# Performance work log

Hardware: AMD Instinct MI355X
Metric: run time of the kernel (lower is better)

Reference implementation:

```python
import jax, jax.numpy as jnp
import numpy as np

N_NODES = 6000
DEG = 16
N_EDGES = N_NODES * DEG
D_MODEL = 256
D_MSG = 64
D_FF = 4 * D_MODEL
N_LAYERS = 3
N_SPECIES = 108
RBF_BINS = D_MODEL
RBF_VMIN, RBF_VMAX = 0.0, 8.0


def setup_inputs():
    key = jax.random.key(0)
    ks = jax.random.split(key, 16)
    rng = np.random.default_rng(0)
    # graph: each node i has DEG in-edges (dst block-structured), random sources
    atomic_number = jnp.asarray(rng.integers(1, N_SPECIES, N_NODES), dtype=jnp.int32)
    dst = np.repeat(np.arange(N_NODES), DEG)
    src = rng.integers(0, N_NODES, N_EDGES)
    # angle graph t: nodes = edges of g; edges = all ordered pairs of in-edges sharing dst
    pq = np.array([(p, q) for p in range(DEG) for q in range(DEG) if p != q], dtype=np.int64)
    off = (np.arange(N_NODES) * DEG)[:, None]
    t_src = (off + pq[:, 0][None, :]).reshape(-1)
    t_dst = (off + pq[:, 1][None, :]).reshape(-1)
    r = jax.random.normal(ks[0], (N_EDGES, 3), dtype=jnp.float32) * 2.0  # bond vectors, |r|~3A
    s_dm = 1.0 / np.sqrt(D_MODEL)
    s_dmsg = 1.0 / np.sqrt(D_MSG)
    s_ff = 1.0 / np.sqrt(D_FF)
    return {
        'r': r,
        'atomic_number': atomic_number,
        'src': jnp.asarray(src, dtype=jnp.int32),
        'dst': jnp.asarray(dst, dtype=jnp.int32),
        't_src': jnp.asarray(t_src, dtype=jnp.int32),
        't_dst': jnp.asarray(t_dst, dtype=jnp.int32),
        'emb': jax.random.normal(ks[1], (N_SPECIES, D_MODEL), dtype=jnp.float32),
        'Wsrc': jax.random.normal(ks[2], (N_LAYERS, D_MSG, D_MODEL), dtype=jnp.float32) * s_dm,
        'bsrc': jnp.zeros((N_LAYERS, D_MSG), jnp.float32),
        'Wdst': jax.random.normal(ks[3], (N_LAYERS, D_MSG, D_MODEL), dtype=jnp.float32) * s_dm,
        'bdst': jnp.zeros((N_LAYERS, D_MSG), jnp.float32),
        'Wedge': jax.random.normal(ks[4], (N_LAYERS, D_MSG, D_MODEL), dtype=jnp.float32) * s_dm,
        'bedge': jnp.zeros((N_LAYERS, D_MSG), jnp.float32),
        'attn': jax.random.normal(ks[5], (N_LAYERS, D_MSG), dtype=jnp.float32) * s_dmsg,
        'W1': jax.random.normal(ks[6], (N_LAYERS, D_FF, D_MSG), dtype=jnp.float32) * s_dmsg,
        'b1': jnp.zeros((N_LAYERS, D_FF), jnp.float32),
        'W2': jax.random.normal(ks[7], (N_LAYERS, D_MODEL, D_FF), dtype=jnp.float32) * s_ff,
        'b2': jnp.zeros((N_LAYERS, D_MODEL), jnp.float32),
        'Wfc': jax.random.normal(ks[8], (1, D_MODEL), dtype=jnp.float32) * s_dm,
        'bfc': jnp.zeros((1,), jnp.float32),
    }


def _segment_softmax(logits, seg, num):
    m = jax.ops.segment_max(logits, seg, num_segments=num)
    ex = jnp.exp(logits - m[seg])
    z = jax.ops.segment_sum(ex, seg, num_segments=num)
    return ex / z[seg]


def reference(r, atomic_number, src, dst, t_src, t_dst, emb, Wsrc, bsrc, Wdst, bdst,
              Wedge, bedge, attn, W1, b1, W2, b2, Wfc, bfc):
    x = emb[atomic_number]                                   # [N, d_model]
    d = jnp.linalg.norm(r, axis=1)                           # [E]
    centers = jnp.linspace(RBF_VMIN, RBF_VMAX, RBF_BINS, dtype=r.dtype)
    gamma = 1.0 / (centers[1] - centers[0])
    y = jnp.exp(-gamma * (d[:, None] - centers[None, :]) ** 2)  # [E, d_model]
    rhat = r / d[:, None]
    # cos angle between edge pairs (sign of -r cancels in u_dot_v)
    cos_jik = jnp.clip(jnp.sum(rhat[t_src] * rhat[t_dst], axis=1), -1.0 + 1e-6, 1.0 - 1e-6)
    nch = jnp.arange(D_MSG, dtype=r.dtype)
    z_jik = jnp.cos(nch[None, :] * jnp.arccos(cos_jik)[:, None])  # Chebyshev T_k(cos) [T, 64]
    for l in range(N_LAYERS):
        xj = x @ Wsrc[l].T + bsrc[l]                          # [N, 64]
        xi = x @ Wdst[l].T + bdst[l]
        xij = xj[src] + xi[dst] + (y @ Wedge[l].T + bedge[l])  # [E, 64]
        e_jik = jax.nn.silu(z_jik + xij[t_src] + xij[t_dst])   # [T, 64]
        logits = e_jik @ attn[l]                               # [T]
        a = _segment_softmax(logits, t_dst, N_EDGES)           # edge_softmax over angle graph
        ft = jax.ops.segment_sum(a[:, None] * xij[t_src], t_dst, num_segments=N_EDGES)  # [E, 64]
        xn = jax.ops.segment_sum(ft, dst, num_segments=N_NODES)  # scatter to nodes [N, 64]
        x = jax.nn.silu(xn @ W1[l].T + b1[l]) @ W2[l].T + b2[l]  # FFN -> [N, d_model]
    atomwise = x @ Wfc.T + bfc                                  # [N, 1]
    return jnp.squeeze(jnp.mean(atomwise, axis=0))              # AvgPooling (eV/atom)


if __name__ == '__main__':
    out = reference(**setup_inputs())
    print(out)
```

## Files before the change

### kernel.cpp

```cpp
#include <hip/hip_runtime.h>

#define N_NODES 6000
#define DEG_    16
#define N_EDGES (N_NODES*DEG_)
#define D_MODEL 256
#define D_MSG   64
#define D_FF    1024

typedef __bf16 bf16x8 __attribute__((ext_vector_type(8)));
typedef float floatx4 __attribute__((ext_vector_type(4)));

__device__ __forceinline__ float silu_f(float v) {
    return v * __builtin_amdgcn_rcpf(1.0f + __expf(-v));
}
__device__ __forceinline__ float b2f(unsigned short u) {
    union { unsigned int i; float f; } v; v.i = ((unsigned int)u) << 16; return v.f;
}
__device__ __forceinline__ unsigned short f2b(float f) {
    union { float f; unsigned int i; } v; v.f = f;
    unsigned int r = (v.i + 0x7FFFu + ((v.i >> 16) & 1u)) >> 16;
    return (unsigned short)r;
}

#define WSRC_OFF 0
#define WDST_OFF 49152
#define WCVT_TOTAL 98304
#define CVT4_BLOCKS (WCVT_TOTAL/4/256)
#define EMB4_BLOCKS (N_NODES*D_MODEL/4/256)
#define GEOM_BLOCKS (N_EDGES/256)
#define WPACKE_BLOCKS 24
#define WPACK1_BLOCKS 96
__global__ __launch_bounds__(256) void prep_kernel(
    const float* __restrict__ Wsrc, const float* __restrict__ Wdst,
    const float* __restrict__ Wedge, const float* __restrict__ W1,
    unsigned short* __restrict__ wbf_out,
    const int* __restrict__ an, const float* __restrict__ emb,
    unsigned short* __restrict__ x,
    const float* __restrict__ r, float* __restrict__ d, float* __restrict__ rhat,
    unsigned short* __restrict__ wedgep,
    unsigned short* __restrict__ w1p) {
    int b = blockIdx.x;
    int t = threadIdx.x;
    if (b < CVT4_BLOCKS) {
        int i = (b*256 + t) * 4;
        const float* sp = (i < WDST_OFF) ? (Wsrc + i) : (Wdst + (i - WDST_OFF));
        float4 v = *(const float4*)sp;
        *(ushort4*)(wbf_out + i) = make_ushort4(f2b(v.x), f2b(v.y), f2b(v.z), f2b(v.w));
    } else if (b < CVT4_BLOCKS + EMB4_BLOCKS) {
        int i4 = (b - CVT4_BLOCKS)*256 + t;
        int node = i4 >> 6, c4 = i4 & 63;
        float4 v = *(const float4*)(emb + (size_t)an[node]*D_MODEL + c4*4);
        *(ushort4*)(x + (size_t)node*D_MODEL + c4*4) =
            make_ushort4(f2b(v.x), f2b(v.y), f2b(v.z), f2b(v.w));
    } else if (b < CVT4_BLOCKS + EMB4_BLOCKS + GEOM_BLOCKS) {
        int e = (b - CVT4_BLOCKS - EMB4_BLOCKS)*256 + t;
        float xx = r[e*3+0], yy = r[e*3+1], zz = r[e*3+2];
        float n = sqrtf(xx*xx + yy*yy + zz*zz);
        d[e] = n;
        float inv = 1.0f / n;
        *(float4*)(rhat + (size_t)e*4) = make_float4(xx*inv, yy*inv, zz*inv, 0.f);
    } else if (b < CVT4_BLOCKS + EMB4_BLOCKS + GEOM_BLOCKS + WPACKE_BLOCKS) {
        int wb = b - (CVT4_BLOCKS + EMB4_BLOCKS + GEOM_BLOCKS);
        int i = wb*256 + t;
        int lane = i & 63, ks = (i >> 6) & 7, rem = i >> 9;
        int ns = rem % 3, w = rem / 3;
        int row = 48*w + ns*16 + (lane & 15);
        int col = ks*32 + (lane >> 4)*8;
        const float* sp = Wedge + (size_t)row*256 + col;
        float4 v0 = *(const float4*)sp;
        float4 v1 = *(const float4*)(sp + 4);
        unsigned short h[8] = { f2b(v0.x), f2b(v0.y), f2b(v0.z), f2b(v0.w),
                                f2b(v1.x), f2b(v1.y), f2b(v1.z), f2b(v1.w) };
        *(uint4*)(wedgep + (size_t)i*8) = *(uint4*)h;
    } else {
        int wb = b - (CVT4_BLOCKS + EMB4_BLOCKS + GEOM_BLOCKS + WPACKE_BLOCKS);
        int i2 = wb*256 + t;
        int lp = i2 >> 13;
        int e = i2 & 8191;
        int lane = e & 63, j = (e >> 6) & 1, wv = (e >> 7) & 3, f = e >> 9;
        int row = f*64 + wv*16 + (lane & 15);
        int col = j*32 + (lane >> 4)*8;
        const float* sp = W1 + (size_t)lp*65536 + (size_t)row*64 + col;
        float4 v0 = *(const float4*)sp;
        float4 v1 = *(const float4*)(sp + 4);
        unsigned short h[8] = { f2b(v0.x), f2b(v0.y), f2b(v0.z), f2b(v0.w),
                                f2b(v1.x), f2b(v1.y), f2b(v1.z), f2b(v1.w) };
        *(uint4*)(w1p + (size_t)i2*8) = *(uint4*)h;
    }
}

#define EPITCH 264
#define APITCH 40
#define MCP 72
__global__ __launch_bounds__(256) void eplg_kernel(
    const unsigned short* __restrict__ Bwp,
    const float* __restrict__ bias,
    const float* __restrict__ dvec,
    unsigned short* __restrict__ C,
    const unsigned short* __restrict__ A,
    const unsigned short* __restrict__ B1g,
    const unsigned short* __restrict__ B2g,
    const float* __restrict__ bias1,
    const float* __restrict__ bias2,
    unsigned short* __restrict__ Cg,
    const float* __restrict__ Wsrc, const float* __restrict__ Wdst,
    const float* __restrict__ W2, const float* __restrict__ b2,
    const float* __restrict__ Wfc, const float* __restrict__ bfc,
    unsigned short* __restrict__ wcomb,
    float* __restrict__ bcomb,
    float* __restrict__ wfc2,
    float* __restrict__ out) {
    __shared__ __align__(16) unsigned short sm[64*EPITCH];
    const int t = threadIdx.x;
    const int w = t >> 6, lane = t & 63, lr = lane & 15, lq = lane >> 4;

    if (blockIdx.x < 1500) {
        unsigned short* As = sm;
        const int m0 = blockIdx.x * 64;
        const int arow = t >> 2, achk = t & 3;

        float dv = dvec[m0 + arow];
        const float gamma = 31.875f;
        const float step  = 8.0f / 255.0f;
        #pragma unroll
        for (int c32 = 0; c32 < 8; ++c32) {
            int kb = c32*32 + achk*8;
            unsigned short h[8];
            #pragma unroll
            for (int j = 0; j < 8; ++j) {
                float tt = dv - (float)(kb+j)*step;
                h[j] = f2b(__expf(-gamma*tt*tt));
            }
            *(uint4*)(&As[arow*EPITCH + kb]) = *(uint4*)h;
        }
        __syncthreads();

        const unsigned short* Bp = Bwp + (size_t)w*12288 + lane*8;

        floatx4 acc[4][3] = {};
        uint4 pb[3];
        #pragma unroll
        for (int ns = 0; ns < 3; ++ns)
            pb[ns] = *(const uint4*)(Bp + ns*4096);

        for (int k0 = 0; k0 < 256; k0 += 32) {
            int ks = k0 >> 5;
            uint4 cb[3];
            cb[0] = pb[0]; cb[1] = pb[1]; cb[2] = pb[2];
            if (k0 + 32 < 256) {
                #pragma unroll
                for (int ns = 0; ns < 3; ++ns)
                    pb[ns] = *(const uint4*)(Bp + ns*4096 + (ks+1)*512);
            }
            bf16x8 af[4];
            #pragma unroll
            for (int mi = 0; mi < 4; ++mi)
                af[mi] = *(const bf16x8*)(&As[(mi*16 + lr)*EPITCH + k0 + lq*8]);
            #pragma unroll
            for (int mi = 0; mi < 4; ++mi) {
                #pragma unroll
                for (int ns = 0; ns < 3; ++ns)
                    acc[mi][ns] = __builtin_amdgcn_mfma_f32_16x16x32_bf16(
                        af[mi], *(const bf16x8*)&cb[ns], acc[mi][ns], 0, 0, 0);
            }
        }

        #pragma unroll
        for (int ns = 0; ns < 3; ++ns) {
            int bc = 48*w + ns*16 + lr;
            float bv = bias[bc];
            #pragma unroll
            for (int mi = 0; mi < 4; ++mi) {
                #pragma unroll
                for (int rg = 0; rg < 4; ++rg) {
                    int row = m0 + mi*16 + lq*4 + rg;
                    C[(size_t)row*192 + bc] = f2b(acc[mi][ns][rg] + bv);
                }
            }
        }
        return;
    }
    if (blockIdx.x < 1688) {
        unsigned short* As = sm;
        unsigned short* Bs = sm + 2560;
        unsigned short* Cs = sm;
        const int bid2 = blockIdx.x - 1500;
        const int bx = bid2 & 1;
        const int m0 = (bid2 >> 1) * 64;
        const unsigned short* B = bx ? B2g : B1g;
        const float* biasl = bx ? bias2 : bias1;
        const int n0 = bx * 64;
        const int K = 256, M = N_NODES, lda = 256, ldb = 256, ldc = 128;

        const int arow = t >> 2, achk = t & 3;

        floatx4 acc[4] = {};
        uint4 pa, pb;
        {
            int gm = m0 + arow;
            pa = (gm < M) ? *(const uint4*)(A + (size_t)gm*lda + achk*8) : make_uint4(0,0,0,0);
        }
        pb = *(const uint4*)(B + (size_t)arow*ldb + achk*8);

        for (int k0 = 0; k0 < K; k0 += 32) {
            *(uint4*)(&As[arow*APITCH + achk*8]) = pa;
            *(uint4*)(&Bs[arow*APITCH + achk*8]) = pb;
            __syncthreads();
            if (k0 + 32 < K) {
                int kn = k0 + 32;
                int gm = m0 + arow;
                pa = (gm < M) ? *(const uint4*)(A + (size_t)gm*lda + kn + achk*8) : make_uint4(0,0,0,0);
                pb = *(const uint4*)(B + (size_t)arow*ldb + kn + achk*8);
            }
            bf16x8 af, bfr[4];
            af = *(const bf16x8*)(&As[(w*16 + lr)*APITCH + lq*8]);
            #pragma unroll
            for (int ns = 0; ns < 4; ++ns)
                bfr[ns] = *(const bf16x8*)(&Bs[(ns*16 + lr)*APITCH + lq*8]);
            #pragma unroll
            for (int ns = 0; ns < 4; ++ns)
                acc[ns] = __builtin_amdgcn_mfma_f32_16x16x32_bf16(af, bfr[ns], acc[ns], 0,0,0);
            __syncthreads();
        }
        #pragma unroll
        for (int ns = 0; ns < 4; ++ns) {
            int bc = ns*16 + lr;
            float bv = biasl[bc];
            #pragma unroll
            for (int rg = 0; rg < 4; ++rg) {
                int lrow = w*16 + lq*4 + rg;
                Cs[lrow*MCP + bc] = f2b(acc[ns][rg] + bv);
            }
        }
        __syncthreads();
        #pragma unroll
        for (int it = 0; it < 2; ++it) {
            int i = t + it*256;
            int row = i >> 3, c8 = i & 7;
            int gm = m0 + row;
            if (gm < M)
                *(uint4*)(Cg + (size_t)gm*ldc + n0 + c8*8) = *(const uint4*)(Cs + row*MCP + c8*8);
        }
        return;
    }
    {
        int b = blockIdx.x - 1688;
        if (b < 64) {
            int lp  = 1 + (b >> 5);
            int wb2 = b & 31;
            const float* W2f = W2 + (size_t)(lp-1)*262144;
            const float* wm[4];
            #pragma unroll
            for (int i = 0; i < 4; ++i) {
                int row = wb2*4 + i;
                wm[i] = (row < 64) ? (Wsrc + (size_t)lp*16384 + row*256)
                                   : (Wdst + (size_t)lp*16384 + (row-64)*256);
            }
            float acc[4][4] = {};
            int c0 = t*4;
            #pragma unroll 8
            for (int c = 0; c < 256; ++c) {
                float4 w2v = *(const float4*)(W2f + (size_t)c*1024 + c0);
                #pragma unroll
                for (int i = 0; i < 4; ++i) {
                    float wv2 = wm[i][c];
                    acc[i][0] = fmaf(wv2, w2v.x, acc[i][0]);
                    acc[i][1] = fmaf(wv2, w2v.y, acc[i][1]);
                    acc[i][2] = fmaf(wv2, w2v.z, acc[i][2]);
                    acc[i][3] = fmaf(wv2, w2v.w, acc[i][3]);
                }
            }
            int fc = t >> 4, j = (t >> 3) & 1, lq2 = (t >> 1) & 3, cpos = (t & 1) * 4;
            #pragma unroll
            for (int i = 0; i < 4; ++i) {
                int row = wb2*4 + i;
                int wv2 = row >> 5, ns = (row >> 4) & 1, lr2 = row & 15;
                *(ushort4*)(wcomb + (size_t)(lp-1)*131072
                            + (size_t)fc*8192 + wv2*2048 + ns*1024 + j*512 + (lq2*16+lr2)*8 + cpos) =
                    make_ushort4(f2b(acc[i][0]), f2b(acc[i][1]), f2b(acc[i][2]), f2b(acc[i][3]));
            }
        } else if (b < 68) {
            int c = (b - 64)*256 + t;
            const float* W2f = W2 + 2*262144;
            float a0 = 0.f, a1 = 0.f, a2 = 0.f, a3 = 0.f;
            #pragma unroll 4
            for (int k = 0; k < 256; k += 4) {
                a0 = fmaf(Wfc[k+0], W2f[(size_t)(k+0)*1024 + c], a0);
                a1 = fmaf(Wfc[k+1], W2f[(size_t)(k+1)*1024 + c], a1);
                a2 = fmaf(Wfc[k+2], W2f[(size_t)(k+2)*1024 + c], a2);
                a3 = fmaf(Wfc[k+3], W2f[(size_t)(k+3)*1024 + c], a3);
            }
            wfc2[c] = (a0 + a1) + (a2 + a3);
        } else {
            int lp = 1 + (t >> 7);
            int row = t & 127;
            const float* b2l = b2 + (lp-1)*256;
            const float* wmrow = (row < 64) ? (Wsrc + (size_t)lp*16384 + row*256)
                                            : (Wdst + (size_t)lp*16384 + (row-64)*256);
            float acc = 0.f;
            #pragma unroll 8
            for (int c = 0; c < 256; ++c) acc += wmrow[c] * b2l[c];
            acc += (row < 64) ? bias1[lp*64 + row] : bias2[lp*64 + (row-64)];
            bcomb[(lp-1)*128 + row] = acc;
            if (t == 0) {
                float bo = 0.f;
                const float* b23 = b2 + 2*256;
                #pragma unroll 8
                for (int c = 0; c < 256; ++c) bo += Wfc[c] * b23[c];
                out[0] = bo + bfc[0];
            }
        }
    }
}

#define HP 72
#define CP2 136
__global__ __launch_bounds__(256) void ffw_kernel(
    const unsigned short* __restrict__ XN,
    const unsigned short* __restrict__ W1p,
    const float* __restrict__ b1l,
    const unsigned short* __restrict__ WCp,
    const float* __restrict__ bcl,
    unsigned short* __restrict__ XO,
    int M) {
    __shared__ __align__(16) unsigned short s_h[16*HP];
    __shared__ __align__(16) unsigned short s_c[16*CP2];
    const int t = threadIdx.x;
    const int wv = t >> 6, lane = t & 63, lr = lane & 15, lq = lane >> 4;
    const int m0 = blockIdx.x * 16;

    int ga = m0 + lr;
    bool aok = ga < M;
    uint4 a0 = aok ? *(const uint4*)(XN + (size_t)ga*64 + lq*8) : make_uint4(0,0,0,0);
    uint4 a1 = aok ? *(const uint4*)(XN + (size_t)ga*64 + 32 + lq*8) : make_uint4(0,0,0,0);

    floatx4 acc2[2] = {};

    const unsigned short* W1b = W1p + (size_t)wv*1024 + lane*8;
    const unsigned short* WCb = WCp + (size_t)wv*2048 + lane*8;

    uint4 pb1[2], pb2[4];
    pb1[0] = *(const uint4*)(W1b);
    pb1[1] = *(const uint4*)(W1b + 512);
    pb2[0] = *(const uint4*)(WCb);
    pb2[1] = *(const uint4*)(WCb + 512);
    pb2[2] = *(const uint4*)(WCb + 1024);
    pb2[3] = *(const uint4*)(WCb + 1536);

    for (int f = 0; f < 16; ++f) {
        uint4 cb1_0 = pb1[0], cb1_1 = pb1[1];
        uint4 cb2_0 = pb2[0], cb2_1 = pb2[1], cb2_2 = pb2[2], cb2_3 = pb2[3];
        float bv1 = b1l[f*64 + wv*16 + lr];
        if (f < 15) {
            const unsigned short* n1 = W1b + (f+1)*4096;
            const unsigned short* n2 = WCb + (f+1)*8192;
            pb1[0] = *(const uint4*)(n1);
            pb1[1] = *(const uint4*)(n1 + 512);
            pb2[0] = *(const uint4*)(n2);
            pb2[1] = *(const uint4*)(n2 + 512);
            pb2[2] = *(const uint4*)(n2 + 1024);
            pb2[3] = *(const uint4*)(n2 + 1536);
        }
        floatx4 hacc = {};
        hacc = __builtin_amdgcn_mfma_f32_16x16x32_bf16(
            *(const bf16x8*)&a0, *(const bf16x8*)&cb1_0, hacc, 0,0,0);
        hacc = __builtin_amdgcn_mfma_f32_16x16x32_bf16(
            *(const bf16x8*)&a1, *(const bf16x8*)&cb1_1, hacc, 0,0,0);
        {
            int col = wv*16 + lr;
            #pragma unroll
            for (int rg = 0; rg < 4; ++rg) {
                int row = lq*4 + rg;
                s_h[row*HP + col] = f2b(silu_f(hacc[rg] + bv1));
            }
        }
        __syncthreads();
        bf16x8 ha0 = *(const bf16x8*)(&s_h[lr*HP + lq*8]);
        bf16x8 ha1 = *(const bf16x8*)(&s_h[lr*HP + 32 + lq*8]);
        acc2[0] = __builtin_amdgcn_mfma_f32_16x16x32_bf16(ha0, *(const bf16x8*)&cb2_0, acc2[0], 0,0,0);
        acc2[0] = __builtin_amdgcn_mfma_f32_16x16x32_bf16(ha1, *(const bf16x8*)&cb2_1, acc2[0], 0,0,0);
        acc2[1] = __builtin_amdgcn_mfma_f32_16x16x32_bf16(ha0, *(const bf16x8*)&cb2_2, acc2[1], 0,0,0);
        acc2[1] = __builtin_amdgcn_mfma_f32_16x16x32_bf16(ha1, *(const bf16x8*)&cb2_3, acc2[1], 0,0,0);
        __syncthreads();
    }

    #pragma unroll
    for (int ns = 0; ns < 2; ++ns) {
        int col = wv*32 + ns*16 + lr;
        float bv = bcl[col];
        #pragma unroll
        for (int rg = 0; rg < 4; ++rg) {
            int row = lq*4 + rg;
            s_c[row*CP2 + col] = f2b(acc2[ns][rg] + bv);
        }
    }
    __syncthreads();
    {
        int row = t >> 4, c8 = t & 15;
        int gm = m0 + row;
        if (gm < M)
            *(uint4*)(XO + (size_t)gm*128 + c8*8) = *(const uint4*)(s_c + row*CP2 + c8*8);
    }
}

__global__ __launch_bounds__(256) void ffa_kernel(
    const unsigned short* __restrict__ XN,
    const unsigned short* __restrict__ W1p,
    const float* __restrict__ b1l,
    const float* __restrict__ wfc2,
    float* __restrict__ out, int M) {
    __shared__ float red[256];
    const int t = threadIdx.x;
    const int wv = t >> 6, lane = t & 63, lr = lane & 15, lq = lane >> 4;
    const int m0 = blockIdx.x * 16;

    int ga = m0 + lr;
    bool aok = ga < M;
    uint4 a0 = aok ? *(const uint4*)(XN + (size_t)ga*64 + lq*8) : make_uint4(0,0,0,0);
    uint4 a1 = aok ? *(const uint4*)(XN + (size_t)ga*64 + 32 + lq*8) : make_uint4(0,0,0,0);

    const unsigned short* W1b = W1p + (size_t)wv*1024 + lane*8;
    uint4 pb0 = *(const uint4*)(W1b);
    uint4 pb1 = *(const uint4*)(W1b + 512);

    float partial = 0.f;
    for (int f = 0; f < 16; ++f) {
        uint4 c0 = pb0, c1 = pb1;
        if (f < 15) {
            pb0 = *(const uint4*)(W1b + (f+1)*4096);
            pb1 = *(const uint4*)(W1b + (f+1)*4096 + 512);
        }
        floatx4 hacc = {};
        hacc = __builtin_amdgcn_mfma_f32_16x16x32_bf16(
            *(const bf16x8*)&a0, *(const bf16x8*)&c0, hacc, 0,0,0);
        hacc = __builtin_amdgcn_mfma_f32_16x16x32_bf16(
            *(const bf16x8*)&a1, *(const bf16x8*)&c1, hacc, 0,0,0);
        float bv1 = b1l[f*64 + wv*16 + lr];
        float wvv = wfc2[f*64 + wv*16 + lr];
        #pragma unroll
        for (int rg = 0; rg < 4; ++rg) {
            int gm = m0 + lq*4 + rg;
            if (gm < M) partial += silu_f(hacc[rg] + bv1) * wvv;
        }
    }
    red[t] = partial;
    __syncthreads();
    for (int off = 128; off > 0; off >>= 1) {
        if (t < off) red[t] += red[t+off];
        __syncthreads();
    }
    if (t == 0) atomicAdd(out, red[0] * (1.0f/(float)N_NODES));
}

__global__ __launch_bounds__(256) void angle_kernel(
    const unsigned short* __restrict__ xjxi,
    const unsigned short* __restrict__ eproj,
    const float* __restrict__ rhat,
    const int*   __restrict__ src,
    const float* __restrict__ attn,
    unsigned short* __restrict__ xn) {
    __shared__ __align__(16) float s_xij[16][68];
    __shared__ float s_rhat[16][4];
    __shared__ float s_logit[16][17];
    __shared__ float s_a[16][17];
    __shared__ float s_w[16];
    const int tt = threadIdx.x;
    const int node = blockIdx.x;

    if (tt < 16) {
        float4 rv = *(const float4*)(rhat + (size_t)(node*DEG_ + tt)*4);
        s_rhat[tt][0] = rv.x; s_rhat[tt][1] = rv.y; s_rhat[tt][2] = rv.z; s_rhat[tt][3] = 0.f;
        s_logit[tt][tt] = -1e30f;
    }
    {
        int p = tt >> 4, c4 = tt & 15;
        int e = node*DEG_ + p;
        int se = src[e];
        ushort4 aj = *(const ushort4*)(xjxi + (size_t)se*128 + c4*4);
        ushort4 ai = *(const ushort4*)(xjxi + (size_t)node*128 + 64 + c4*4);
        ushort4 ae = *(const ushort4*)(eproj + (size_t)e*192 + c4*4);
        s_xij[p][c4*4+0] = b2f(aj.x) + b2f(ai.x) + b2f(ae.x);
        s_xij[p][c4*4+1] = b2f(aj.y) + b2f(ai.y) + b2f(ae.y);
        s_xij[p][c4*4+2] = b2f(aj.z) + b2f(ai.z) + b2f(ae.z);
        s_xij[p][c4*4+3] = b2f(aj.w) + b2f(ai.w) + b2f(ae.w);
    }
    __syncthreads();
    int pp = 0, qq = 0;
    float lg = 0.f;
    if (tt < 240) {
        int pair = tt >> 1, half = tt & 1;
        pp = (int)((1.0f + sqrtf(8.0f*(float)pair + 1.0f)) * 0.5f);
        qq = pair - ((pp*(pp-1)) >> 1);
        float c = s_rhat[pp][0]*s_rhat[qq][0] + s_rhat[pp][1]*s_rhat[qq][1]
                + s_rhat[pp][2]*s_rhat[qq][2];
        c = fminf(fmaxf(c, -0.999999f), 0.999999f);
        float c2 = 2.0f * c;
        float tk0, tk1;
        if (half) {
            float T2  = fmaf(c2, c, -1.0f);
            float T3  = fmaf(2.0f*T2,  c,   -c);
            float T4  = fmaf(2.0f*T2,  T2,  -1.0f);
            float T7  = fmaf(2.0f*T4,  T3,  -c);
            float T8  = fmaf(2.0f*T4,  T4,  -1.0f);
            float T15 = fmaf(2.0f*T8,  T7,  -c);
            float T16 = fmaf(2.0f*T8,  T8,  -1.0f);
            float T31 = fmaf(2.0f*T16, T15, -c);
            float T32 = fmaf(2.0f*T16, T16, -1.0f);
            float T33 = fmaf(2.0f*T32, c,   -T31);
            tk0 = T32; tk1 = T33;
        } else {
            tk0 = 1.0f; tk1 = c;
        }
        const float* xp = &s_xij[pp][0] + half*32;
        const float* xq = &s_xij[qq][0] + half*32;
        const float* at = attn + half*32;
        float acc = 0.f;
        #pragma unroll
        for (int k0 = 0; k0 < 32; k0 += 4) {
            float4 xp4 = *(const float4*)(xp + k0);
            float4 xq4 = *(const float4*)(xq + k0);
            float a0 = at[k0+0], a1 = at[k0+1], a2 = at[k0+2], a3 = at[k0+3];
            float v0 = tk0 + xp4.x + xq4.x;
            acc = fmaf(a0, silu_f(v0), acc);
            { float tn2 = c2*tk1 - tk0; tk0 = tk1; tk1 = tn2; }
            float v1 = tk0 + xp4.y + xq4.y;
            acc = fmaf(a1, silu_f(v1), acc);
            { float tn2 = c2*tk1 - tk0; tk0 = tk1; tk1 = tn2; }
            float v2 = tk0 + xp4.z + xq4.z;
            acc = fmaf(a2, silu_f(v2), acc);
            { float tn2 = c2*tk1 - tk0; tk0 = tk1; tk1 = tn2; }
            float v3 = tk0 + xp4.w + xq4.w;
            acc = fmaf(a3, silu_f(v3), acc);
            { float tn2 = c2*tk1 - tk0; tk0 = tk1; tk1 = tn2; }
        }
        lg = acc;
    }
    lg += __shfl_xor(lg, 1);
    if (tt < 240 && (tt & 1) == 0) {
        s_logit[pp][qq] = lg;
        s_logit[qq][pp] = lg;
    }
    __syncthreads();
    {
        int q = tt >> 4, p = tt & 15;
        float l = s_logit[p][q];
        float m = l;
        m = fmaxf(m, __shfl_xor(m, 1));
        m = fmaxf(m, __shfl_xor(m, 2));
        m = fmaxf(m, __shfl_xor(m, 4));
        m = fmaxf(m, __shfl_xor(m, 8));
        float e = __expf(l - m);
        float z = e;
        z += __shfl_xor(z, 1);
        z += __shfl_xor(z, 2);
        z += __shfl_xor(z, 4);
        z += __shfl_xor(z, 8);
        s_a[p][q] = e * __builtin_amdgcn_rcpf(z);
    }
    __syncthreads();
    {
        int p = tt >> 4, q = tt & 15;
        float a = s_a[p][q];
        a += __shfl_xor(a, 1);
        a += __shfl_xor(a, 2);
        a += __shfl_xor(a, 4);
        a += __shfl_xor(a, 8);
        if (q == 0) s_w[p] = a;
    }
    __syncthreads();
    if (tt < 64) {
        float acc = 0.f;
        #pragma unroll
        for (int p = 0; p < 16; ++p) acc += s_w[p] * s_xij[p][tt];
        xn[(size_t)node*64 + tt] = f2b(acc);
    }
}

extern "C" void kernel_launch(void* const* d_in, const int* in_sizes, int n_in,
                              void* d_out, int out_size, void* d_ws, size_t ws_size,
                              hipStream_t stream) {
    (void)in_sizes; (void)n_in; (void)out_size; (void)ws_size;
    const float* r    = (const float*)d_in[0];
    const int*   an   = (const int*)  d_in[1];
    const int*   src  = (const int*)  d_in[2];
    const float* emb  = (const float*)d_in[6];
    const float* Wsrc = (const float*)d_in[7];
    const float* bsrc = (const float*)d_in[8];
    const float* Wdst = (const float*)d_in[9];
    const float* bdst = (const float*)d_in[10];
    const float* Wedge= (const float*)d_in[11];
    const float* bedge= (const float*)d_in[12];
    const float* attn = (const float*)d_in[13];
    const float* W1   = (const float*)d_in[14];
    const float* b1   = (const float*)d_in[15];
    const float* W2   = (const float*)d_in[16];
    const float* b2   = (const float*)d_in[17];
    const float* Wfc  = (const float*)d_in[18];
    const float* bfc  = (const float*)d_in[19];

    char* ws = (char*)d_ws;
    float* d_d              = (float*)(ws);
    float* d_rhat           = (float*)(ws + 384000);
    unsigned short* wbf     = (unsigned short*)(ws + 1920000);
    unsigned short* d_x     = (unsigned short*)(ws + 4180992);
    unsigned short* d_xjxi  = (unsigned short*)(ws + 7252992);
    unsigned short* d_eproj = (unsigned short*)(ws + 8788992);
    unsigned short* d_xn    = (unsigned short*)(ws + 45652992);
    unsigned short* d_wcomb = (unsigned short*)(ws + 46420992);
    float* d_bcomb          = (float*)(ws + 46945280);
    float* d_wfc2           = (float*)(ws + 46946304);
    unsigned short* d_wedgep= (unsigned short*)(ws + 46950400);
    unsigned short* d_w1p   = (unsigned short*)(ws + 47048704);
    float* out = (float*)d_out;

    unsigned short* wsrc_bf  = wbf + WSRC_OFF;
    unsigned short* wdst_bf  = wbf + WDST_OFF;

    prep_kernel<<<CVT4_BLOCKS + EMB4_BLOCKS + GEOM_BLOCKS + WPACKE_BLOCKS + WPACK1_BLOCKS,
                  256, 0, stream>>>(
        Wsrc, Wdst, Wedge, W1, wbf, an, emb, d_x, r, d_d, d_rhat, d_wedgep, d_w1p);

    eplg_kernel<<<1500 + 188 + 69, 256, 0, stream>>>(
        d_wedgep, bedge, d_d, d_eproj,
        d_x, wsrc_bf, wdst_bf, bsrc, bdst, d_xjxi,
        Wsrc, Wdst, W2, b2, Wfc, bfc,
        d_wcomb, d_bcomb, d_wfc2, out);

    angle_kernel<<<N_NODES, 256, 0, stream>>>(
        d_xjxi, d_eproj, d_rhat, src, attn, d_xn);
    ffw_kernel<<<375, 256, 0, stream>>>(
        d_xn, d_w1p, b1, d_wcomb, d_bcomb, d_xjxi, N_NODES);

    angle_kernel<<<N_NODES, 256, 0, stream>>>(
        d_xjxi, d_eproj + 64, d_rhat, src, attn + 64, d_xn);
    ffw_kernel<<<375, 256, 0, stream>>>(
        d_xn, d_w1p + 65536, b1 + 1024, d_wcomb + 131072, d_bcomb + 128, d_xjxi, N_NODES);

    angle_kernel<<<N_NODES, 256, 0, stream>>>(
        d_xjxi, d_eproj + 128, d_rhat, src, attn + 128, d_xn);
    ffa_kernel<<<375, 256, 0, stream>>>(
        d_xn, d_w1p + 131072, b1 + 2048, d_wfc2, out, N_NODES);
}
```

Before: 229.4 us.

## Generate RBF A-fragments in registers and split edge GEMM by rows per wave

The edge-feature GEMM blocks no longer stage the RBF-expanded A tile in LDS. Each wave now computes its own 16-row A fragments directly in registers and loops over all 12 output column tiles, loading B per tile. This removes the LDS write, the barrier and the LDS reads, and it shrinks the shared memory allocation, which may raise occupancy. In exchange, each wave now reads all of B rather than a quarter of it, which raises global/L2 traffic for the weights.

```diff
diff --git a/kernel.cpp b/kernel.cpp
--- a/kernel.cpp
+++ b/kernel.cpp
@@ -89,7 +89,6 @@
     }
 }
 
-#define EPITCH 264
 #define APITCH 40
 #define MCP 72
 __global__ __launch_bounds__(256) void eplg_kernel(
@@ -110,72 +109,46 @@
     float* __restrict__ bcomb,
     float* __restrict__ wfc2,
     float* __restrict__ out) {
-    __shared__ __align__(16) unsigned short sm[64*EPITCH];
+    __shared__ __align__(16) unsigned short sm[5120];
     const int t = threadIdx.x;
     const int w = t >> 6, lane = t & 63, lr = lane & 15, lq = lane >> 4;
 
     if (blockIdx.x < 1500) {
-        unsigned short* As = sm;
         const int m0 = blockIdx.x * 64;
-        const int arow = t >> 2, achk = t & 3;
-
-        float dv = dvec[m0 + arow];
+        float dv = dvec[m0 + w*16 + lr];
         const float gamma = 31.875f;
         const float step  = 8.0f / 255.0f;
-        #pragma unroll
-        for (int c32 = 0; c32 < 8; ++c32) {
-            int kb = c32*32 + achk*8;
+        bf16x8 af[8];
+        #pragma unroll
+        for (int ks = 0; ks < 8; ++ks) {
             unsigned short h[8];
+            int kb = ks*32 + lq*8;
             #pragma unroll
             for (int j = 0; j < 8; ++j) {
-                float tt = dv - (float)(kb+j)*step;
-                h[j] = f2b(__expf(-gamma*tt*tt));
-            }
-            *(uint4*)(&As[arow*EPITCH + kb]) = *(uint4*)h;
-        }
-        __syncthreads();
-
-        const unsigned short* Bp = Bwp + (size_t)w*12288 + lane*8;
-
-        floatx4 acc[4][3] = {};
-        uint4 pb[3];
-        #pragma unroll
-        for (int ns = 0; ns < 3; ++ns)
-            pb[ns] = *(const uint4*)(Bp + ns*4096);
-
-        for (int k0 = 0; k0 < 256; k0 += 32) {
-            int ks = k0 >> 5;
-            uint4 cb[3];
-            cb[0] = pb[0]; cb[1] = pb[1]; cb[2] = pb[2];
-            if (k0 + 32 < 256) {
-                #pragma unroll
-                for (int ns = 0; ns < 3; ++ns)
-                    pb[ns] = *(const uint4*)(Bp + ns*4096 + (ks+1)*512);
-            }
-            bf16x8 af[4];
-            #pragma unroll
-            for (int mi = 0; mi < 4; ++mi)
-                af[mi] = *(const bf16x8*)(&As[(mi*16 + lr)*EPITCH + k0 + lq*8]);
-            #pragma unroll
-            for (int mi = 0; mi < 4; ++mi) {
-                #pragma unroll
-                for (int ns = 0; ns < 3; ++ns)
-                    acc[mi][ns] = __builtin_amdgcn_mfma_f32_16x16x32_bf16(
-                        af[mi], *(const bf16x8*)&cb[ns], acc[mi][ns], 0, 0, 0);
-            }
-        }
-
-        #pragma unroll
-        for (int ns = 0; ns < 3; ++ns) {
-            int bc = 48*w + ns*16 + lr;
+                float tt2 = dv - (float)(kb+j)*step;
+                h[j] = f2b(__expf(-gamma*tt2*tt2));
+            }
+            af[ks] = *(bf16x8*)h;
+        }
+        const unsigned short* Bl = Bwp + lane*8;
+        #pragma unroll
+        for (int ct = 0; ct < 12; ++ct) {
+            const unsigned short* Bb = Bl + (ct/3)*12288 + (ct%3)*4096;
+            uint4 pb[8];
+            #pragma unroll
+            for (int ks = 0; ks < 8; ++ks)
+                pb[ks] = *(const uint4*)(Bb + ks*512);
+            floatx4 acc = {};
+            #pragma unroll
+            for (int ks = 0; ks < 8; ++ks)
+                acc = __builtin_amdgcn_mfma_f32_16x16x32_bf16(
+                    af[ks], *(const bf16x8*)&pb[ks], acc, 0, 0, 0);
+            int bc = (ct/3)*48 + (ct%3)*16 + lr;
             float bv = bias[bc];
             #pragma unroll
-            for (int mi = 0; mi < 4; ++mi) {
-                #pragma unroll
-                for (int rg = 0; rg < 4; ++rg) {
-                    int row = m0 + mi*16 + lq*4 + rg;
-                    C[(size_t)row*192 + bc] = f2b(acc[mi][ns][rg] + bv);
-                }
+            for (int rg = 0; rg < 4; ++rg) {
+                int row = m0 + w*16 + lq*4 + rg;
+                C[(size_t)row*192 + bc] = f2b(acc[rg] + bv);
             }
         }
         return;
```

Result: no change. 231.9 us (+1.1%).
